# Kernel tuning notes

Measured on AMD Instinct MI355X. Metric: run time of the kernel, lower is better.

## Reference

```python
import jax, jax.numpy as jnp
import numpy as np

N_NODES = 2000
BATCH = 512
N_TOTAL = BATCH * N_NODES
NUM_FEAT = 16
HID = 8
OUT = 8
N_EDGES = 16 * N_TOTAL
SLOPE = 0.01


def _leaky(v):
    return jax.nn.leaky_relu(v, SLOPE)


def setup_inputs() -> dict:
    key = jax.random.key(0)
    ks = jax.random.split(key, 24)
    inp = {
        "x": jax.random.normal(ks[0], (N_TOTAL, NUM_FEAT), dtype=jnp.float32),
        "edge_index": jax.random.randint(ks[1], (2, N_EDGES), 0, N_TOTAL, dtype=jnp.int32),
        "batch_size": BATCH,
    }
    def lin(k, fi, fo):
        return jax.random.normal(k, (fi, fo), dtype=jnp.float32) * (1.0 / np.sqrt(fi))
    dims = [(NUM_FEAT, HID), (HID, HID), (HID, HID), (HID, OUT)]
    i = 2
    for l, (fi, fo) in enumerate(dims):
        inp[f"w{l}a"] = lin(ks[i], fi, fo); i += 1
        inp[f"b{l}a"] = jax.random.normal(ks[i], (fo,), dtype=jnp.float32) * 0.02; i += 1
        inp[f"w{l}b"] = lin(ks[i], fo, fo); i += 1
        inp[f"b{l}b"] = jax.random.normal(ks[i], (fo,), dtype=jnp.float32) * 0.02; i += 1
    inp["fc1_w"] = lin(ks[i], OUT, 1); i += 1
    inp["fc1_b"] = jax.random.normal(ks[i], (1,), dtype=jnp.float32) * 0.02; i += 1
    inp["fc2_w"] = lin(ks[i], N_NODES, 2); i += 1
    inp["fc2_b"] = jax.random.normal(ks[i], (2,), dtype=jnp.float32) * 0.02
    return inp


def _gin_conv(h, src, dst, wa, ba, wb, bb):
    # GINConv (eps=0): MLP((1+eps)*x + sum_{j in N(i)} x_j)
    agg = h + jax.ops.segment_sum(h[src], dst, num_segments=h.shape[0])
    return _leaky(agg @ wa + ba) @ wb + bb  # MLP: Lin -> LeakyReLU -> Lin


def reference(x, edge_index, batch_size,
              w0a, b0a, w0b, b0b, w1a, b1a, w1b, b1b,
              w2a, b2a, w2b, b2b, w3a, b3a, w3b, b3b,
              fc1_w, fc1_b, fc2_w, fc2_b):
    src, dst = edge_index[0], edge_index[1]
    h = _gin_conv(x, src, dst, w0a, b0a, w0b, b0b)
    h = _leaky(h)  # inter-layer act (dropout is eval-mode identity)
    h = _gin_conv(h, src, dst, w1a, b1a, w1b, b1b)
    h = _leaky(h)
    h = _gin_conv(h, src, dst, w2a, b2a, w2b, b2b)
    h = _leaky(h)
    h = _gin_conv(h, src, dst, w3a, b3a, w3b, b3b)  # no act after last conv
    n_nodes = h.shape[0] // batch_size
    h = h.reshape(batch_size, n_nodes, h.shape[-1])       # [B, n, out_ch]
    z = _leaky(h) @ fc1_w + fc1_b                         # [B, n, 1]
    z = z.reshape(batch_size, n_nodes)                    # [B, n]
    z = _leaky(z) @ fc2_w + fc2_b                         # [B, 2]
    return jax.nn.log_softmax(z, axis=1)
```

## Files before the change

kernel.cpp:

```cpp
#include <hip/hip_runtime.h>

#define N_TOTAL 1024000
#define N_EDGES 16384000
#define SLOPE 0.01f
#define NBUCK 4000
#define BCAP  5120
#define NCOARSE 250
#define CCAP 73472
#define CTILE 4096

__device__ __forceinline__ float lrelu(float v){ return v > 0.0f ? v : SLOPE*v; }


__global__ void __launch_bounds__(256) k_init(const float* __restrict__ x,
                       const float* __restrict__ w,
                       float* __restrict__ P){
  int i = blockIdx.x*256 + threadIdx.x;
  if (i >= N_TOTAL) return;
  const float4* xr = (const float4*)(x + (size_t)i*16);
  float4 a0 = xr[0], a1 = xr[1], a2 = xr[2], a3 = xr[3];
  float xi[16] = {a0.x,a0.y,a0.z,a0.w, a1.x,a1.y,a1.z,a1.w,
                  a2.x,a2.y,a2.z,a2.w, a3.x,a3.y,a3.z,a3.w};
  float p[8];
  #pragma unroll
  for (int j=0;j<8;j++){
    float s = 0.f;
    #pragma unroll
    for (int k=0;k<16;k++) s += xi[k]*w[k*8+j];
    p[j] = s;
  }
  float4* Pr = (float4*)(P + (size_t)i*8);
  Pr[0] = make_float4(p[0],p[1],p[2],p[3]);
  Pr[1] = make_float4(p[4],p[5],p[6],p[7]);
}

__global__ void __launch_bounds__(256) k_mid(float* __restrict__ P, const float* __restrict__ Q,
                      const float* __restrict__ wb, const float* __restrict__ bb,
                      const float* __restrict__ wa){
  int i = blockIdx.x*256 + threadIdx.x;
  if (i >= N_TOTAL) return;
  const float4* Qr = (const float4*)(Q + (size_t)i*8);
  float4 q0 = Qr[0], q1 = Qr[1];
  float g[8] = {lrelu(q0.x),lrelu(q0.y),lrelu(q0.z),lrelu(q0.w),
                lrelu(q1.x),lrelu(q1.y),lrelu(q1.z),lrelu(q1.w)};
  float h[8];
  #pragma unroll
  for (int j=0;j<8;j++){
    float s = bb[j];
    #pragma unroll
    for (int k=0;k<8;k++) s += g[k]*wb[k*8+j];
    h[j] = lrelu(s);
  }
  float p[8];
  #pragma unroll
  for (int j=0;j<8;j++){
    float s = 0.f;
    #pragma unroll
    for (int k=0;k<8;k++) s += h[k]*wa[k*8+j];
    p[j] = s;
  }
  float4* Pr = (float4*)(P + (size_t)i*8);
  Pr[0] = make_float4(p[0],p[1],p[2],p[3]);
  Pr[1] = make_float4(p[4],p[5],p[6],p[7]);
}

__global__ void __launch_bounds__(256) k_part1(const int* __restrict__ src, const int* __restrict__ dst,
                                               int* __restrict__ cntC, int* __restrict__ coarse){
  __shared__ int ebuf[CTILE];
  __shared__ unsigned char bkt[CTILE];
  __shared__ int hist[256], tmp[256], exS[256], delta[256];
  int tid = threadIdx.x;
  int tileBase = blockIdx.x * CTILE;
  hist[tid] = 0;
  __syncthreads();
  int pay[16]; int rnk[16]; int bk[16];
  #pragma unroll
  for (int k=0;k<16;k++){
    int idx = tileBase + k*256 + tid;
    int d = dst[idx], s = src[idx];
    int b = d >> 12;
    pay[k] = ((d & 4095) << 20) | s;
    bk[k] = b;
    rnk[k] = atomicAdd(&hist[b], 1);
  }
  __syncthreads();
  int v = hist[tid];
  tmp[tid] = v; __syncthreads();
  for (int off=1; off<256; off<<=1){
    int t2 = (tid>=off) ? tmp[tid-off] : 0; __syncthreads();
    tmp[tid] += t2; __syncthreads();
  }
  int ex = tmp[tid] - v;
  exS[tid] = ex;
  if (tid < NCOARSE && v > 0){
    int g = atomicAdd(&cntC[tid], v);
    delta[tid] = g - ex;
  }
  __syncthreads();
  #pragma unroll
  for (int k=0;k<16;k++){
    int p = exS[bk[k]] + rnk[k];
    ebuf[p] = pay[k];
    bkt[p] = (unsigned char)bk[k];
  }
  __syncthreads();
  for (int i = tid; i < CTILE; i += 256){
    int b = bkt[i];
    int lp = delta[b] + i;
    if ((unsigned)lp < CCAP) coarse[b*CCAP + lp] = ebuf[i];
  }
}

__global__ void __launch_bounds__(256) k_part2(const int* __restrict__ coarse, const int* __restrict__ cntC,
                                               int* __restrict__ cntF, int* __restrict__ packed){
  __shared__ int ebuf[CTILE];
  __shared__ unsigned char bkt[CTILE];
  __shared__ int hist[16], tmp16[16], exS[16], delta[16];
  int tid = threadIdx.x;
  int c = blockIdx.x;
  int n = cntC[c]; if (n > CCAP) n = CCAP;
  int tileBase = blockIdx.y * CTILE;
  if (tileBase >= n) return;
  int cntE = n - tileBase; if (cntE > CTILE) cntE = CTILE;
  if (tid < 16) hist[tid] = 0;
  __syncthreads();
  unsigned pay[16]; int rnk[16]; int bk[16];
  const int* reg = coarse + (size_t)c*CCAP + tileBase;
  #pragma unroll
  for (int k=0;k<16;k++){
    int idx = k*256 + tid;
    bk[k] = -1;
    if (idx < cntE){
      unsigned e = (unsigned)reg[idx];
      int f = (int)(e >> 28);
      pay[k] = e & 0x0FFFFFFFu;
      bk[k] = f;
      rnk[k] = atomicAdd(&hist[f], 1);
    }
  }
  __syncthreads();
  if (tid < 16) tmp16[tid] = hist[tid];
  __syncthreads();
  for (int off=1; off<16; off<<=1){
    int t2 = 0;
    if (tid < 16 && tid >= off) t2 = tmp16[tid-off];
    __syncthreads();
    if (tid < 16) tmp16[tid] += t2;
    __syncthreads();
  }
  if (tid < 16){
    int vv = hist[tid];
    int ex = tmp16[tid] - vv;
    exS[tid] = ex;
    if (vv > 0) delta[tid] = atomicAdd(&cntF[c*16 + tid], vv) - ex;
  }
  __syncthreads();
  #pragma unroll
  for (int k=0;k<16;k++){
    if (bk[k] >= 0){
      int p = exS[bk[k]] + rnk[k];
      ebuf[p] = (int)pay[k];
      bkt[p] = (unsigned char)bk[k];
    }
  }
  __syncthreads();
  for (int i = tid; i < cntE; i += 256){
    int f = bkt[i];
    int lp = delta[f] + i;
    if ((unsigned)lp < BCAP) packed[(size_t)(c*16 + f)*BCAP + lp] = ebuf[i];
  }
}

__global__ void __launch_bounds__(256) k_bin(const int* __restrict__ src, const int* __restrict__ dst,
                                             int* __restrict__ cnt, int* __restrict__ packed){
  int t = blockIdx.x*256 + threadIdx.x;
  if (t >= N_EDGES) return;
  int d = dst[t], s = src[t];
  int b = d >> 8, l = d & 255;
  int p = atomicAdd(&cnt[b], 1);
  if (p < BCAP) packed[b*BCAP + p] = (l << 20) | s;
}

__global__ void __launch_bounds__(256) k_csr(int* __restrict__ packed, const int* __restrict__ cnt,
                                             int2* __restrict__ row2){
  __shared__ int ebuf[BCAP];
  __shared__ int hist[256], pos[256], tmp[256];
  int b = blockIdx.x, tid = threadIdx.x;
  int n = cnt[b]; if (n > BCAP) n = BCAP;
  int* region = packed + (size_t)b*BCAP;
  hist[tid] = 0;
  __syncthreads();
  for (int i = tid; i < n; i += 256){
    int e = region[i];
    ebuf[i] = e;
    atomicAdd(&hist[e >> 20], 1);
  }
  __syncthreads();
  int v = hist[tid];
  tmp[tid] = v; __syncthreads();
  for (int off=1; off<256; off<<=1){
    int t2 = (tid>=off) ? tmp[tid-off] : 0; __syncthreads();
    tmp[tid] += t2; __syncthreads();
  }
  int ex = tmp[tid] - v;
  pos[tid] = ex;
  int base = b*BCAP;
  row2[b*256 + tid] = make_int2(base + ex, base + ex + v);
  __syncthreads();
  for (int i = tid; i < n; i += 256){
    int e = ebuf[i];
    int l = e >> 20, s = e & 0xFFFFF;
    int p = atomicAdd(&pos[l], 1);
    region[p] = s;
  }
}

__global__ void __launch_bounds__(256) k_agg(const float* __restrict__ P,
                                             const int2* __restrict__ row2,
                                             const int* __restrict__ csr,
                                             const float* __restrict__ b,
                                             float* __restrict__ Q){
  int t = blockIdx.x*256 + threadIdx.x;
  int node = t >> 3;
  int j = t & 7;
  if (node >= N_TOTAL) return;
  int2 r = row2[node];
  float acc = P[(size_t)node*8 + j] + b[j];
  int e = r.x;
  for (; e+3 < r.y; e += 4){
    int s0 = csr[e], s1 = csr[e+1], s2 = csr[e+2], s3 = csr[e+3];
    float v0 = P[(size_t)s0*8 + j];
    float v1 = P[(size_t)s1*8 + j];
    float v2 = P[(size_t)s2*8 + j];
    float v3 = P[(size_t)s3*8 + j];
    acc += v0; acc += v1; acc += v2; acc += v3;
  }
  for (; e < r.y; e++) acc += P[(size_t)csr[e]*8 + j];
  Q[(size_t)node*8 + j] = acc;
}

__global__ void __launch_bounds__(256) k_qinit(const float* __restrict__ P, const float* __restrict__ b,
                                               float* __restrict__ Q){
  int t = blockIdx.x*256 + threadIdx.x;
  if (t < N_TOTAL*8) Q[t] = P[t] + b[t & 7];
}

__global__ void __launch_bounds__(256) k_scatter(const int* __restrict__ src,
                                                 const int* __restrict__ dst,
                                                 const float* __restrict__ P,
                                                 float* __restrict__ Q){
  int t = blockIdx.x*256 + threadIdx.x;
  int e = t >> 3;
  int j = t & 7;
  int s = src[e];
  int d = dst[e];
  float v = P[(size_t)s*8 + j];
  atomicAdd(Q + (size_t)d*8 + j, v);
}

__global__ void __launch_bounds__(256) k_readout(const float* __restrict__ Q,
                          const float* __restrict__ wb, const float* __restrict__ bb,
                          const float* __restrict__ fc1w, const float* __restrict__ fc1b,
                          const float* __restrict__ fc2w, const float* __restrict__ fc2b,
                          float* __restrict__ out){
  int bi = blockIdx.x;
  int tid = threadIdx.x;
  float acc0 = 0.f, acc1 = 0.f;
  for (int n = tid; n < 2000; n += 256){
    size_t i = (size_t)bi*2000 + n;
    const float4* qr = (const float4*)(Q + i*8);
    float4 q0 = qr[0], q1 = qr[1];
    float g[8] = {lrelu(q0.x),lrelu(q0.y),lrelu(q0.z),lrelu(q0.w),
                  lrelu(q1.x),lrelu(q1.y),lrelu(q1.z),lrelu(q1.w)};
    float s = fc1b[0];
    #pragma unroll
    for (int j=0;j<8;j++){
      float h = bb[j];
      #pragma unroll
      for (int k=0;k<8;k++) h += g[k]*wb[k*8+j];
      s += lrelu(h)*fc1w[j];
    }
    float t = lrelu(s);
    acc0 += t*fc2w[n*2+0];
    acc1 += t*fc2w[n*2+1];
  }
  #pragma unroll
  for (int off = 32; off > 0; off >>= 1){
    acc0 += __shfl_down(acc0, off);
    acc1 += __shfl_down(acc1, off);
  }
  __shared__ float s0[4], s1[4];
  int w = tid >> 6;
  if ((tid & 63) == 0){ s0[w] = acc0; s1[w] = acc1; }
  __syncthreads();
  if (tid == 0){
    float z0 = s0[0]+s0[1]+s0[2]+s0[3] + fc2b[0];
    float z1 = s1[0]+s1[1]+s1[2]+s1[3] + fc2b[1];
    float m = fmaxf(z0, z1);
    float lse = m + logf(expf(z0-m) + expf(z1-m));
    out[bi*2+0] = z0 - lse;
    out[bi*2+1] = z1 - lse;
  }
}

extern "C" void kernel_launch(void* const* d_in, const int* in_sizes, int n_in,
                              void* d_out, int out_size, void* d_ws, size_t ws_size,
                              hipStream_t stream){
  const float* x   = (const float*)d_in[0];
  const int*   ei  = (const int*)d_in[1];
  const int*   src = ei;
  const int*   dst = ei + N_EDGES;
  const float* w0a=(const float*)d_in[3],  *b0a=(const float*)d_in[4];
  const float* w0b=(const float*)d_in[5],  *b0b=(const float*)d_in[6];
  const float* w1a=(const float*)d_in[7],  *b1a=(const float*)d_in[8];
  const float* w1b=(const float*)d_in[9],  *b1b=(const float*)d_in[10];
  const float* w2a=(const float*)d_in[11], *b2a=(const float*)d_in[12];
  const float* w2b=(const float*)d_in[13], *b2b=(const float*)d_in[14];
  const float* w3a=(const float*)d_in[15], *b3a=(const float*)d_in[16];
  const float* w3b=(const float*)d_in[17], *b3b=(const float*)d_in[18];
  const float* fc1w=(const float*)d_in[19],*fc1b=(const float*)d_in[20];
  const float* fc2w=(const float*)d_in[21],*fc2b=(const float*)d_in[22];
  float* out = (float*)d_out;

  char* base = (char*)d_ws;
  float* P      = (float*)base;  base += (size_t)N_TOTAL*8*4;
  float* Q      = (float*)base;  base += (size_t)N_TOTAL*8*4;
  size_t atomic_need = (size_t)(base - (char*)d_ws);
  int2*  row2   = (int2*)base;   base += (size_t)N_TOTAL*8;
  int*   cnt    = (int*)base;    base += 4096*4;
  int*   packed = (int*)base;    base += (size_t)NBUCK*BCAP*4;
  size_t need = (size_t)(base - (char*)d_ws);

  int* coarse = (int*)P;
  int* cntC   = coarse + (size_t)NCOARSE*CCAP;

  const int nb_nodes = (N_TOTAL + 255)/256;
  const int nb_edges = (N_EDGES + 255)/256;
  const int nb_nf    = (N_TOTAL*8 + 255)/256;

  if (ws_size >= need){
    hipMemsetAsync(cnt, 0, (size_t)NBUCK*4, stream);
    hipMemsetAsync(cntC, 0, (size_t)NCOARSE*4, stream);
    k_part1<<<N_EDGES/CTILE,256,0,stream>>>(src, dst, cntC, coarse);
    dim3 g2(NCOARSE, (CCAP + CTILE - 1)/CTILE);
    k_part2<<<g2,256,0,stream>>>(coarse, cntC, cnt, packed);
    k_csr<<<NBUCK,256,0,stream>>>(packed, cnt, row2);

    k_init<<<nb_nodes,256,0,stream>>>(x, w0a, P);
    k_agg <<<nb_nf,256,0,stream>>>(P, row2, packed, b0a, Q);
    k_mid <<<nb_nodes,256,0,stream>>>(P, Q, w0b, b0b, w1a);
    k_agg <<<nb_nf,256,0,stream>>>(P, row2, packed, b1a, Q);
    k_mid <<<nb_nodes,256,0,stream>>>(P, Q, w1b, b1b, w2a);
    k_agg <<<nb_nf,256,0,stream>>>(P, row2, packed, b2a, Q);
    k_mid <<<nb_nodes,256,0,stream>>>(P, Q, w2b, b2b, w3a);
    k_agg <<<nb_nf,256,0,stream>>>(P, row2, packed, b3a, Q);
  } else if (ws_size >= atomic_need){
    k_init<<<nb_nodes,256,0,stream>>>(x, w0a, P);
    k_qinit<<<nb_nf,256,0,stream>>>(P, b0a, Q);
    k_scatter<<<(N_EDGES*8)/256,256,0,stream>>>(src,dst,P,Q);
    k_mid <<<nb_nodes,256,0,stream>>>(P, Q, w0b, b0b, w1a);
    k_qinit<<<nb_nf,256,0,stream>>>(P, b1a, Q);
    k_scatter<<<(N_EDGES*8)/256,256,0,stream>>>(src,dst,P,Q);
    k_mid <<<nb_nodes,256,0,stream>>>(P, Q, w1b, b1b, w2a);
    k_qinit<<<nb_nf,256,0,stream>>>(P, b2a, Q);
    k_scatter<<<(N_EDGES*8)/256,256,0,stream>>>(src,dst,P,Q);
    k_mid <<<nb_nodes,256,0,stream>>>(P, Q, w2b, b2b, w3a);
    k_qinit<<<nb_nf,256,0,stream>>>(P, b3a, Q);
    k_scatter<<<(N_EDGES*8)/256,256,0,stream>>>(src,dst,P,Q);
  }
  k_readout<<<512,256,0,stream>>>(Q,w3b,b3b,fc1w,fc1b,fc2w,fc2b,out);
}
```

Before: 1.590 ms.

## Fuse per-layer MLP into CSR aggregation and gather edges with float4 lanes

The aggregation kernel is rewritten so each node's 8 lanes split into 2 feature halves and 4 edge groups. Each lane gathers float4 rows and the partial sums are combined with cross-lane shuffles. For the first three layers the following MLP step (LeakyReLU, second linear, activation, next layer's first linear) runs inside the same kernel, which removes the separate k_mid launches and the round trip of the intermediate Q through global memory. Ping-ponging between P and Q avoids in-place hazards, at the cost of more register pressure and idle lanes during the dense MLP tail.

```diff
diff --git a/kernel.cpp b/kernel.cpp
--- a/kernel.cpp
+++ b/kernel.cpp
@@ -10,6 +10,13 @@
 #define CTILE 4096
 
 __device__ __forceinline__ float lrelu(float v){ return v > 0.0f ? v : SLOPE*v; }
+__device__ __forceinline__ float4 f4add(float4 a, float4 b){
+  return make_float4(a.x+b.x, a.y+b.y, a.z+b.z, a.w+b.w);
+}
+__device__ __forceinline__ float4 shfl_xor4(float4 v, int m){
+  return make_float4(__shfl_xor(v.x,m), __shfl_xor(v.y,m),
+                     __shfl_xor(v.z,m), __shfl_xor(v.w,m));
+}
 
 
 __global__ void __launch_bounds__(256) k_init(const float* __restrict__ x,
@@ -171,16 +178,6 @@
   }
 }
 
-__global__ void __launch_bounds__(256) k_bin(const int* __restrict__ src, const int* __restrict__ dst,
-                                             int* __restrict__ cnt, int* __restrict__ packed){
-  int t = blockIdx.x*256 + threadIdx.x;
-  if (t >= N_EDGES) return;
-  int d = dst[t], s = src[t];
-  int b = d >> 8, l = d & 255;
-  int p = atomicAdd(&cnt[b], 1);
-  if (p < BCAP) packed[b*BCAP + p] = (l << 20) | s;
-}
-
 __global__ void __launch_bounds__(256) k_csr(int* __restrict__ packed, const int* __restrict__ cnt,
                                              int2* __restrict__ row2){
   __shared__ int ebuf[BCAP];
@@ -215,28 +212,78 @@
   }
 }
 
-__global__ void __launch_bounds__(256) k_agg(const float* __restrict__ P,
-                                             const int2* __restrict__ row2,
-                                             const int* __restrict__ csr,
-                                             const float* __restrict__ b,
-                                             float* __restrict__ Q){
+template<int FUSE>
+__global__ void __launch_bounds__(256) k_aggf(const float* __restrict__ Pin,
+                                              const int2* __restrict__ row2,
+                                              const int* __restrict__ csr,
+                                              const float* __restrict__ bias,
+                                              const float* __restrict__ wb,
+                                              const float* __restrict__ bb,
+                                              const float* __restrict__ wa,
+                                              float* __restrict__ Out){
   int t = blockIdx.x*256 + threadIdx.x;
-  int node = t >> 3;
-  int j = t & 7;
-  if (node >= N_TOTAL) return;
+  int node = t >> 3, l = t & 7;
+  int half = l & 1, eo = l >> 1;
   int2 r = row2[node];
-  float acc = P[(size_t)node*8 + j] + b[j];
-  int e = r.x;
-  for (; e+3 < r.y; e += 4){
-    int s0 = csr[e], s1 = csr[e+1], s2 = csr[e+2], s3 = csr[e+3];
-    float v0 = P[(size_t)s0*8 + j];
-    float v1 = P[(size_t)s1*8 + j];
-    float v2 = P[(size_t)s2*8 + j];
-    float v3 = P[(size_t)s3*8 + j];
-    acc += v0; acc += v1; acc += v2; acc += v3;
-  }
-  for (; e < r.y; e++) acc += P[(size_t)csr[e]*8 + j];
-  Q[(size_t)node*8 + j] = acc;
+  float4 acc;
+  if (l < 2){
+    float4 own = *(const float4*)(Pin + (size_t)node*8 + half*4);
+    acc = make_float4(own.x + bias[half*4+0], own.y + bias[half*4+1],
+                      own.z + bias[half*4+2], own.w + bias[half*4+3]);
+  } else {
+    acc = make_float4(0.f,0.f,0.f,0.f);
+  }
+  for (int e = r.x; e < r.y; e += 8){
+    int i0 = e + eo, i1 = e + 4 + eo;
+    if (i0 < r.y){
+      int s0 = csr[i0];
+      acc = f4add(acc, *(const float4*)(Pin + (size_t)s0*8 + half*4));
+    }
+    if (i1 < r.y){
+      int s1 = csr[i1];
+      acc = f4add(acc, *(const float4*)(Pin + (size_t)s1*8 + half*4));
+    }
+  }
+  acc = f4add(acc, shfl_xor4(acc, 2));
+  acc = f4add(acc, shfl_xor4(acc, 4));
+  if (l >= 2) return;
+  if (!FUSE){
+    *(float4*)(Out + (size_t)node*8 + half*4) = acc;
+    return;
+  }
+  float g0 = lrelu(acc.x), g1 = lrelu(acc.y), g2 = lrelu(acc.z), g3 = lrelu(acc.w);
+  float o0 = __shfl_xor(g0,1), o1 = __shfl_xor(g1,1), o2 = __shfl_xor(g2,1), o3 = __shfl_xor(g3,1);
+  float gl[8];
+  gl[half*4+0]=g0; gl[half*4+1]=g1; gl[half*4+2]=g2; gl[half*4+3]=g3;
+  gl[(1-half)*4+0]=o0; gl[(1-half)*4+1]=o1; gl[(1-half)*4+2]=o2; gl[(1-half)*4+3]=o3;
+  float h[4];
+  #pragma unroll
+  for (int jj=0;jj<4;jj++){
+    int j = half*4 + jj;
+    float s = bb[j];
+    #pragma unroll
+    for (int k=0;k<8;k++) s += gl[k]*wb[k*8+j];
+    h[jj] = lrelu(s);
+  }
+  float ho0 = __shfl_xor(h[0],1), ho1 = __shfl_xor(h[1],1), ho2 = __shfl_xor(h[2],1), ho3 = __shfl_xor(h[3],1);
+  float hl[8];
+  hl[half*4+0]=h[0]; hl[half*4+1]=h[1]; hl[half*4+2]=h[2]; hl[half*4+3]=h[3];
+  hl[(1-half)*4+0]=ho0; hl[(1-half)*4+1]=ho1; hl[(1-half)*4+2]=ho2; hl[(1-half)*4+3]=ho3;
+  float4 p;
+  {
+    int j = half*4;
+    float s0=0.f,s1=0.f,s2=0.f,s3=0.f;
+    #pragma unroll
+    for (int k=0;k<8;k++){
+      float hv = hl[k];
+      s0 += hv*wa[k*8+j+0];
+      s1 += hv*wa[k*8+j+1];
+      s2 += hv*wa[k*8+j+2];
+      s3 += hv*wa[k*8+j+3];
+    }
+    p = make_float4(s0,s1,s2,s3);
+  }
+  *(float4*)(Out + (size_t)node*8 + half*4) = p;
 }
 
 __global__ void __launch_bounds__(256) k_qinit(const float* __restrict__ P, const float* __restrict__ b,
@@ -335,7 +382,6 @@
   int* cntC   = coarse + (size_t)NCOARSE*CCAP;
 
   const int nb_nodes = (N_TOTAL + 255)/256;
-  const int nb_edges = (N_EDGES + 255)/256;
   const int nb_nf    = (N_TOTAL*8 + 255)/256;
 
   if (ws_size >= need){
@@ -347,13 +393,11 @@
     k_csr<<<NBUCK,256,0,stream>>>(packed, cnt, row2);
 
     k_init<<<nb_nodes,256,0,stream>>>(x, w0a, P);
-    k_agg <<<nb_nf,256,0,stream>>>(P, row2, packed, b0a, Q);
-    k_mid <<<nb_nodes,256,0,stream>>>(P, Q, w0b, b0b, w1a);
-    k_agg <<<nb_nf,256,0,stream>>>(P, row2, packed, b1a, Q);
-    k_mid <<<nb_nodes,256,0,stream>>>(P, Q, w1b, b1b, w2a);
-    k_agg <<<nb_nf,256,0,stream>>>(P, row2, packed, b2a, Q);
-    k_mid <<<nb_nodes,256,0,stream>>>(P, Q, w2b, b2b, w3a);
-    k_agg <<<nb_nf,256,0,stream>>>(P, row2, packed, b3a, Q);
+    k_aggf<1><<<nb_nf,256,0,stream>>>(P, row2, packed, b0a, w0b, b0b, w1a, Q);
+    k_aggf<1><<<nb_nf,256,0,stream>>>(Q, row2, packed, b1a, w1b, b1b, w2a, P);
+    k_aggf<1><<<nb_nf,256,0,stream>>>(P, row2, packed, b2a, w2b, b2b, w3a, Q);
+    k_aggf<0><<<nb_nf,256,0,stream>>>(Q, row2, packed, b3a, nullptr, nullptr, nullptr, P);
+    k_readout<<<512,256,0,stream>>>(P, w3b, b3b, fc1w, fc1b, fc2w, fc2b, out);
   } else if (ws_size >= atomic_need){
     k_init<<<nb_nodes,256,0,stream>>>(x, w0a, P);
     k_qinit<<<nb_nf,256,0,stream>>>(P, b0a, Q);
@@ -367,6 +411,6 @@
     k_mid <<<nb_nodes,256,0,stream>>>(P, Q, w2b, b2b, w3a);
     k_qinit<<<nb_nf,256,0,stream>>>(P, b3a, Q);
     k_scatter<<<(N_EDGES*8)/256,256,0,stream>>>(src,dst,P,Q);
-  }
-  k_readout<<<512,256,0,stream>>>(Q,w3b,b3b,fc1w,fc1b,fc2w,fc2b,out);
-}
+    k_readout<<<512,256,0,stream>>>(Q, w3b, b3b, fc1w, fc1b, fc2w, fc2b, out);
+  }
+}
```

Measured after the change: 1.556 ms. 2.1% less time.

## Aggregate per bucket in LDS with source-sorted edges and fuse node MLP

Applied to the files above, without the earlier changes.

The CSR build is replaced by a per-bucket sort on source-node range rather than destination. Aggregation becomes one block per 256-node bucket that accumulates neighbour rows into shared memory with LDS atomics, reading each source row as two float4 loads. The following MLP step (k_mid) is fused into the aggregation kernel's epilogue, which removes three launches and the Q round trip through global memory. The aim is better gather locality and less global traffic, at the cost of shared-memory atomic contention and float summation order that now varies between runs.

```diff
diff --git a/kernel.cpp b/kernel.cpp
--- a/kernel.cpp
+++ b/kernel.cpp
@@ -171,18 +171,7 @@
   }
 }
 
-__global__ void __launch_bounds__(256) k_bin(const int* __restrict__ src, const int* __restrict__ dst,
-                                             int* __restrict__ cnt, int* __restrict__ packed){
-  int t = blockIdx.x*256 + threadIdx.x;
-  if (t >= N_EDGES) return;
-  int d = dst[t], s = src[t];
-  int b = d >> 8, l = d & 255;
-  int p = atomicAdd(&cnt[b], 1);
-  if (p < BCAP) packed[b*BCAP + p] = (l << 20) | s;
-}
-
-__global__ void __launch_bounds__(256) k_csr(int* __restrict__ packed, const int* __restrict__ cnt,
-                                             int2* __restrict__ row2){
+__global__ void __launch_bounds__(256) k_sort(int* __restrict__ packed, const int* __restrict__ cnt){
   __shared__ int ebuf[BCAP];
   __shared__ int hist[256], pos[256], tmp[256];
   int b = blockIdx.x, tid = threadIdx.x;
@@ -193,7 +182,7 @@
   for (int i = tid; i < n; i += 256){
     int e = region[i];
     ebuf[i] = e;
-    atomicAdd(&hist[e >> 20], 1);
+    atomicAdd(&hist[(e & 0xFFFFF) >> 12], 1);
   }
   __syncthreads();
   int v = hist[tid];
@@ -202,41 +191,74 @@
     int t2 = (tid>=off) ? tmp[tid-off] : 0; __syncthreads();
     tmp[tid] += t2; __syncthreads();
   }
-  int ex = tmp[tid] - v;
-  pos[tid] = ex;
-  int base = b*BCAP;
-  row2[b*256 + tid] = make_int2(base + ex, base + ex + v);
+  pos[tid] = tmp[tid] - v;
   __syncthreads();
   for (int i = tid; i < n; i += 256){
     int e = ebuf[i];
-    int l = e >> 20, s = e & 0xFFFFF;
-    int p = atomicAdd(&pos[l], 1);
-    region[p] = s;
-  }
-}
-
-__global__ void __launch_bounds__(256) k_agg(const float* __restrict__ P,
-                                             const int2* __restrict__ row2,
-                                             const int* __restrict__ csr,
-                                             const float* __restrict__ b,
-                                             float* __restrict__ Q){
-  int t = blockIdx.x*256 + threadIdx.x;
-  int node = t >> 3;
-  int j = t & 7;
-  if (node >= N_TOTAL) return;
-  int2 r = row2[node];
-  float acc = P[(size_t)node*8 + j] + b[j];
-  int e = r.x;
-  for (; e+3 < r.y; e += 4){
-    int s0 = csr[e], s1 = csr[e+1], s2 = csr[e+2], s3 = csr[e+3];
-    float v0 = P[(size_t)s0*8 + j];
-    float v1 = P[(size_t)s1*8 + j];
-    float v2 = P[(size_t)s2*8 + j];
-    float v3 = P[(size_t)s3*8 + j];
-    acc += v0; acc += v1; acc += v2; acc += v3;
-  }
-  for (; e < r.y; e++) acc += P[(size_t)csr[e]*8 + j];
-  Q[(size_t)node*8 + j] = acc;
+    int p = atomicAdd(&pos[(e & 0xFFFFF) >> 12], 1);
+    region[p] = e;
+  }
+}
+
+template<int FUSE>
+__global__ void __launch_bounds__(256) k_agg3(const float* __restrict__ Pin,
+                                              const int* __restrict__ packed,
+                                              const int* __restrict__ cnt,
+                                              const float* __restrict__ bias,
+                                              const float* __restrict__ wb,
+                                              const float* __restrict__ bb,
+                                              const float* __restrict__ wa,
+                                              float* __restrict__ Out){
+  __shared__ float Qacc[256*9];
+  int b = blockIdx.x, tid = threadIdx.x;
+  int n = cnt[b]; if (n > BCAP) n = BCAP;
+  const int* region = packed + (size_t)b*BCAP;
+  size_t nodeBase = (size_t)b*256;
+  for (int i = tid; i < 2048; i += 256)
+    Qacc[(i>>3)*9 + (i&7)] = Pin[nodeBase*8 + i] + bias[i&7];
+  __syncthreads();
+  for (int e = tid; e < n; e += 256){
+    int pay = region[e];
+    int l = pay >> 20;
+    int s = pay & 0xFFFFF;
+    const float4* pr = (const float4*)(Pin + (size_t)s*8);
+    float4 v0 = pr[0], v1 = pr[1];
+    float* q = &Qacc[l*9];
+    atomicAdd(q+0, v0.x); atomicAdd(q+1, v0.y);
+    atomicAdd(q+2, v0.z); atomicAdd(q+3, v0.w);
+    atomicAdd(q+4, v1.x); atomicAdd(q+5, v1.y);
+    atomicAdd(q+6, v1.z); atomicAdd(q+7, v1.w);
+  }
+  __syncthreads();
+  size_t o = (nodeBase + tid)*8;
+  if (!FUSE){
+    float4 q0 = make_float4(Qacc[tid*9+0],Qacc[tid*9+1],Qacc[tid*9+2],Qacc[tid*9+3]);
+    float4 q1 = make_float4(Qacc[tid*9+4],Qacc[tid*9+5],Qacc[tid*9+6],Qacc[tid*9+7]);
+    *(float4*)(Out + o)     = q0;
+    *(float4*)(Out + o + 4) = q1;
+    return;
+  }
+  float gl[8];
+  #pragma unroll
+  for (int j=0;j<8;j++) gl[j] = lrelu(Qacc[tid*9+j]);
+  float hl[8];
+  #pragma unroll
+  for (int j=0;j<8;j++){
+    float s = bb[j];
+    #pragma unroll
+    for (int k=0;k<8;k++) s += gl[k]*wb[k*8+j];
+    hl[j] = lrelu(s);
+  }
+  float p[8];
+  #pragma unroll
+  for (int j=0;j<8;j++){
+    float s = 0.f;
+    #pragma unroll
+    for (int k=0;k<8;k++) s += hl[k]*wa[k*8+j];
+    p[j] = s;
+  }
+  *(float4*)(Out + o)     = make_float4(p[0],p[1],p[2],p[3]);
+  *(float4*)(Out + o + 4) = make_float4(p[4],p[5],p[6],p[7]);
 }
 
 __global__ void __launch_bounds__(256) k_qinit(const float* __restrict__ P, const float* __restrict__ b,
@@ -326,7 +348,7 @@
   float* P      = (float*)base;  base += (size_t)N_TOTAL*8*4;
   float* Q      = (float*)base;  base += (size_t)N_TOTAL*8*4;
   size_t atomic_need = (size_t)(base - (char*)d_ws);
-  int2*  row2   = (int2*)base;   base += (size_t)N_TOTAL*8;
+  base += (size_t)N_TOTAL*8;
   int*   cnt    = (int*)base;    base += 4096*4;
   int*   packed = (int*)base;    base += (size_t)NBUCK*BCAP*4;
   size_t need = (size_t)(base - (char*)d_ws);
@@ -335,8 +357,6 @@
   int* cntC   = coarse + (size_t)NCOARSE*CCAP;
 
   const int nb_nodes = (N_TOTAL + 255)/256;
-  const int nb_edges = (N_EDGES + 255)/256;
-  const int nb_nf    = (N_TOTAL*8 + 255)/256;
 
   if (ws_size >= need){
     hipMemsetAsync(cnt, 0, (size_t)NBUCK*4, stream);
@@ -344,17 +364,16 @@
     k_part1<<<N_EDGES/CTILE,256,0,stream>>>(src, dst, cntC, coarse);
     dim3 g2(NCOARSE, (CCAP + CTILE - 1)/CTILE);
     k_part2<<<g2,256,0,stream>>>(coarse, cntC, cnt, packed);
-    k_csr<<<NBUCK,256,0,stream>>>(packed, cnt, row2);
+    k_sort<<<NBUCK,256,0,stream>>>(packed, cnt);
 
     k_init<<<nb_nodes,256,0,stream>>>(x, w0a, P);
-    k_agg <<<nb_nf,256,0,stream>>>(P, row2, packed, b0a, Q);
-    k_mid <<<nb_nodes,256,0,stream>>>(P, Q, w0b, b0b, w1a);
-    k_agg <<<nb_nf,256,0,stream>>>(P, row2, packed, b1a, Q);
-    k_mid <<<nb_nodes,256,0,stream>>>(P, Q, w1b, b1b, w2a);
-    k_agg <<<nb_nf,256,0,stream>>>(P, row2, packed, b2a, Q);
-    k_mid <<<nb_nodes,256,0,stream>>>(P, Q, w2b, b2b, w3a);
-    k_agg <<<nb_nf,256,0,stream>>>(P, row2, packed, b3a, Q);
+    k_agg3<1><<<NBUCK,256,0,stream>>>(P, packed, cnt, b0a, w0b, b0b, w1a, Q);
+    k_agg3<1><<<NBUCK,256,0,stream>>>(Q, packed, cnt, b1a, w1b, b1b, w2a, P);
+    k_agg3<1><<<NBUCK,256,0,stream>>>(P, packed, cnt, b2a, w2b, b2b, w3a, Q);
+    k_agg3<0><<<NBUCK,256,0,stream>>>(Q, packed, cnt, b3a, nullptr, nullptr, nullptr, P);
+    k_readout<<<512,256,0,stream>>>(P, w3b, b3b, fc1w, fc1b, fc2w, fc2b, out);
   } else if (ws_size >= atomic_need){
+    const int nb_nf = (N_TOTAL*8 + 255)/256;
     k_init<<<nb_nodes,256,0,stream>>>(x, w0a, P);
     k_qinit<<<nb_nf,256,0,stream>>>(P, b0a, Q);
     k_scatter<<<(N_EDGES*8)/256,256,0,stream>>>(src,dst,P,Q);
@@ -367,6 +386,6 @@
     k_mid <<<nb_nodes,256,0,stream>>>(P, Q, w2b, b2b, w3a);
     k_qinit<<<nb_nf,256,0,stream>>>(P, b3a, Q);
     k_scatter<<<(N_EDGES*8)/256,256,0,stream>>>(src,dst,P,Q);
-  }
-  k_readout<<<512,256,0,stream>>>(Q,w3b,b3b,fc1w,fc1b,fc2w,fc2b,out);
-}
+    k_readout<<<512,256,0,stream>>>(Q, w3b, b3b, fc1w, fc1b, fc2w, fc2b, out);
+  }
+}
```

After: 3.165 ms. 1.99x slower.
